# Kernel tuning notes

Measured on AMD Instinct MI355X. Metric: run time of the kernel, lower is better.

Reference implementation:

```python
import jax, jax.numpy as jnp
import numpy as np

EPS = 1e-6
D = 1152          # hidden_size
NH_HEADS = 16     # num_attention_heads
HD = D // NH_HEADS
INTER = 4304      # intermediate_size
H4 = 4 * D        # 4608
I4 = 4 * INTER    # 17216
B, H, W = 8, 64, 64
WH, WW = 2, 2


def setup_inputs() -> dict:
    key = jax.random.key(0)
    ks = jax.random.split(key, 12)
    s = 0.02
    inp = {
        "hidden_states": jax.random.normal(ks[0], (B, H * W, D), jnp.float32),
        "tgt_sizes": jnp.full((B, 2), 64, dtype=jnp.int32),
        "attention_mask": jnp.zeros((B, 1, 1, H * W), jnp.float32),
        "ln1_g": jnp.ones((D,), jnp.float32),
        "ln1_b": jnp.zeros((D,), jnp.float32),
        "qkv_w": jax.random.normal(ks[1], (D, 3 * D), jnp.float32) * s,
        "qkv_b": jnp.zeros((3 * D,), jnp.float32),
        "out_w": jax.random.normal(ks[2], (D, D), jnp.float32) * s,
        "out_b": jnp.zeros((D,), jnp.float32),
        "pre_g": jnp.ones((H4,), jnp.float32),
        "pre_b": jnp.zeros((H4,), jnp.float32),
        "w1": jax.random.normal(ks[3], (H4, I4), jnp.float32) * s,
        "b1": jnp.zeros((I4,), jnp.float32),
        "w2": jax.random.normal(ks[4], (I4, D), jnp.float32) * s,
        "b2": jnp.zeros((D,), jnp.float32),
    }
    return inp


def _layernorm(x, g, b):
    m = x.mean(-1, keepdims=True)
    v = ((x - m) ** 2).mean(-1, keepdims=True)
    return (x - m) * jax.lax.rsqrt(v + EPS) * g + b


def _partition(x):
    # x: [B, H*W, D] -> windows [B, nh*nw, wh*ww, D]
    nh, nw = H // WH, W // WW
    x = x.reshape(B, nh, WH, nw, WW, D)
    x = x.transpose(0, 1, 3, 2, 4, 5)  # [B, nh, nw, wh, ww, D]
    return x.reshape(B, nh * nw, WH * WW, D)


def _unpartition(x):
    # windows [B, nh*nw, wh*ww, D] -> [B, H*W, D]
    nh, nw = H // WH, W // WW
    x = x.reshape(B, nh, nw, WH, WW, D)
    x = x.transpose(0, 1, 3, 2, 4, 5)  # [B, nh, wh, nw, ww, D]
    return x.reshape(B, H * W, D)


def reference(hidden_states, tgt_sizes, attention_mask, ln1_g, ln1_b,
              qkv_w, qkv_b, out_w, out_b, pre_g, pre_b, w1, b1, w2, b2):
    nh, nw = H // WH, W // WW
    nwin = nh * nw
    residual = hidden_states
    hs = _layernorm(hidden_states, ln1_g, ln1_b)

    # window self-attention over 4-token windows
    xw = _partition(hs).reshape(B * nwin, WH * WW, D)
    qkv = xw @ qkv_w + qkv_b                               # [N, 4, 3D]
    q, k, v = jnp.split(qkv, 3, axis=-1)
    q = q.reshape(-1, WH * WW, NH_HEADS, HD)
    k = k.reshape(-1, WH * WW, NH_HEADS, HD)
    v = v.reshape(-1, WH * WW, NH_HEADS, HD)
    scale = HD ** -0.5
    scores = jnp.einsum('nqhd,nkhd->nhqk', q, k) * scale
    probs = jax.nn.softmax(scores, axis=-1)
    o = jnp.einsum('nhqk,nkhd->nqhd', probs, v).reshape(-1, WH * WW, D)
    o = o @ out_w + out_b
    attn_out = _unpartition(o.reshape(B, nwin, WH * WW, D))
    hs = residual + attn_out                               # [B, H*W, D]

    # MLP downsample over 2x2 windows
    xw = _partition(hs)                                    # [B, nwin, 4, D]
    res = xw.mean(axis=2)                                  # [B, nwin, D]
    xf = xw.reshape(B, nwin, WH * WW * D)                  # [B, nwin, 4D]
    xf = _layernorm(xf, pre_g, pre_b)
    xf = jax.nn.gelu(xf @ w1 + b1, approximate=True)
    xf = xf @ w2 + b2
    new_hidden = xf + res                                  # [B, nwin, D]

    new_tgt_sizes = tgt_sizes // 2
    # all samples fully valid -> mask of zeros (no -inf positions)
    min_val = jnp.finfo(new_hidden.dtype).min
    valid = jnp.arange(nwin)[None, :] < (new_tgt_sizes[:, 0] * new_tgt_sizes[:, 1])[:, None]
    new_attention_mask = ((~valid).astype(new_hidden.dtype) * min_val)[:, None, None, :]
    return new_hidden, new_tgt_sizes, new_attention_mask
```

## Files before the change

kernel.cpp:

```cpp
#include <hip/hip_runtime.h>
#include <cstdint>
#include <cstddef>

#define DEV __device__ __forceinline__
typedef unsigned short u16;
typedef unsigned int u32;
typedef short bf16x8 __attribute__((ext_vector_type(8)));
typedef float f32x4 __attribute__((ext_vector_type(4)));

typedef __attribute__((address_space(1))) u32 GU32;
typedef __attribute__((address_space(3))) u32 LU32;

DEV float bf2f(u16 v){ u32 x = ((u32)v)<<16; float f; __builtin_memcpy(&f,&x,4); return f; }
DEV u16 f2bf(float f){ u32 x; __builtin_memcpy(&x,&f,4); return (u16)((x + 0x7fffu + ((x>>16)&1u)) >> 16); }

DEV int map_row(int r){
  int b = r>>12, rr = r&4095;
  int win = rr>>2, t = rr&3;
  int wy = win>>5, wx = win&31;
  int y = (wy<<1) + (t>>1), x = (wx<<1) + (t&1);
  return (b<<12) + (y<<6) + x;
}

DEV void gl_lds16(const void* g, void* l){
  __builtin_amdgcn_global_load_lds((const GU32*)g, (LU32*)l, 16, 0, 0);
}

DEV void block_red2(float& s, float& ss, float* red){
  #pragma unroll
  for (int o=32;o;o>>=1){ s += __shfl_down(s,o); ss += __shfl_down(ss,o); }
  const int wv = threadIdx.x>>6;
  if ((threadIdx.x&63)==0){ red[wv*2]=s; red[wv*2+1]=ss; }
  __syncthreads();
  s  = red[0]+red[2]+red[4]+red[6];
  ss = red[1]+red[3]+red[5]+red[7];
}

__launch_bounds__(256)
__global__ void tconv_k(const float* __restrict__ W, u16* __restrict__ WT, int K, int N){
  __shared__ float tl[64][65];
  const int n0 = blockIdx.x << 6, k0 = blockIdx.y << 6;
  const int tx = threadIdx.x & 63, ty = threadIdx.x >> 6;
  #pragma unroll
  for (int rr = 0; rr < 64; rr += 4)
    tl[rr+ty][tx] = W[(size_t)(k0+rr+ty)*N + (n0+tx)];
  __syncthreads();
  #pragma unroll
  for (int rr = 0; rr < 64; rr += 4)
    WT[(size_t)(n0+rr+ty)*K + (k0+tx)] = f2bf(tl[tx][rr+ty]);
}

__launch_bounds__(256)
__global__ void ln1_k(const float* __restrict__ X, const float* __restrict__ g,
                      const float* __restrict__ b, u16* __restrict__ Y){
  __shared__ float red[8];
  const int r = blockIdx.x;
  const float* xr = X + (size_t)map_row(r)*1152;
  const int tid = threadIdx.x;
  const bool has2 = tid < 32;
  float4 v0 = ((const float4*)xr)[tid];
  float4 v1 = {0,0,0,0};
  float s  = v0.x+v0.y+v0.z+v0.w;
  float ss = v0.x*v0.x+v0.y*v0.y+v0.z*v0.z+v0.w*v0.w;
  if (has2){
    v1 = ((const float4*)xr)[tid+256];
    s  += v1.x+v1.y+v1.z+v1.w;
    ss += v1.x*v1.x+v1.y*v1.y+v1.z*v1.z+v1.w*v1.w;
  }
  block_red2(s, ss, red);
  const float mean = s*(1.0f/1152.0f);
  const float rstd = rsqrtf(ss*(1.0f/1152.0f) - mean*mean + 1e-6f);
  u16* yr = Y + (size_t)r*1152;
  {
    float4 gg = ((const float4*)g)[tid];
    float4 bb = ((const float4*)b)[tid];
    ushort4 o;
    o.x = f2bf((v0.x-mean)*rstd*gg.x + bb.x);
    o.y = f2bf((v0.y-mean)*rstd*gg.y + bb.y);
    o.z = f2bf((v0.z-mean)*rstd*gg.z + bb.z);
    o.w = f2bf((v0.w-mean)*rstd*gg.w + bb.w);
    *(ushort4*)(yr + tid*4) = o;
  }
  if (has2){
    float4 gg = ((const float4*)g)[tid+256];
    float4 bb = ((const float4*)b)[tid+256];
    ushort4 o;
    o.x = f2bf((v1.x-mean)*rstd*gg.x + bb.x);
    o.y = f2bf((v1.y-mean)*rstd*gg.y + bb.y);
    o.z = f2bf((v1.z-mean)*rstd*gg.z + bb.z);
    o.w = f2bf((v1.w-mean)*rstd*gg.w + bb.w);
    *(ushort4*)(yr + (tid+256)*4) = o;
  }
}

#define BAR()  asm volatile("s_barrier" ::: "memory")
#define VMW8() asm volatile("s_waitcnt vmcnt(8)" ::: "memory")
#define VMW4() asm volatile("s_waitcnt vmcnt(4)" ::: "memory")
#define VMW0() asm volatile("s_waitcnt vmcnt(0)" ::: "memory")
#define WNONE() do{}while(0)

template<int EPI>
__launch_bounds__(512, 1)
__global__ void gemm8p_k(const u16* __restrict__ A, const u16* __restrict__ BT,
                         int M, int N, int K, int lda, int ldb,
                         void* __restrict__ C, int ldc,
                         const float* __restrict__ bias,
                         const float* __restrict__ aux,
                         int nTM, int nTN)
{
  __shared__ __align__(16) u16 LS[2][2][2][8192];
  const int tid = threadIdx.x;
  const int lane = tid & 63;
  const int wave = tid >> 6;
  const int wr = wave >> 2, wc = wave & 3;

  const int bid  = blockIdx.x;
  const int band = 16 * nTN;
  const int bb   = bid / band, rr_ = bid % band;
  int mcnt = nTM - (bb<<4); if (mcnt > 16) mcnt = 16;
  const int mt = (bb<<4) + rr_ % mcnt;
  const int nt = rr_ / mcnt;
  const int m0 = mt << 8, n0 = nt << 8;

  const int lr1 = tid >> 3, sl = tid & 7;
  const int x_  = sl ^ (lr1 & 7);
  const int grow = ((x_ >> 2) << 7) + lr1;
  const int q_   = x_ & 3;
  const u16* aS = A  + (size_t)(m0 + grow)*lda + q_*8;
  const u16* bS = BT + (size_t)(n0 + grow)*ldb + q_*8;
  const size_t aR64 = (size_t)64*lda, bR64 = (size_t)64*ldb;

  const int l15 = lane & 15, l7 = lane & 7, qh = lane >> 4;
  const int aOff = l15*64 + ((((wr<<2)|qh) ^ l7) << 3);
  const int bOff = ((wc&1)<<12) + l15*64 + (((((wc>>1)<<2)|qh) ^ l7) << 3);

  f32x4 acc[8][4] = {};
  bf16x8 af[4], bv[4];
  const int NT = K >> 6;

#define ST(op_, db_, kh_, t_) do{ \
    const u16* src__ = (op_ ? bS : aS) + (size_t)(t_)*64 + (kh_)*32; \
    u16* dst__ = &LS[(db_)][(op_)][(kh_)][tid*8]; \
    gl_lds16(src__, dst__); \
    gl_lds16(src__ + (op_ ? bR64 : aR64), dst__ + 4096); \
  }while(0)

#define READA(db_, kh_, mh_) do{ \
    const u16* ap__ = &LS[(db_)][0][(kh_)][0] + aOff + ((mh_)?4096:0); \
    _Pragma("unroll") for (int i__=0;i__<4;i__++) af[i__] = *(const bf16x8*)(ap__ + i__*1024); \
  }while(0)

#define READB(db_, kh_) do{ \
    const u16* bp__ = &LS[(db_)][1][(kh_)][0] + bOff; \
    _Pragma("unroll") for (int i__=0;i__<4;i__++) bv[i__] = *(const bf16x8*)(bp__ + i__*1024); \
  }while(0)

#define MFMA16(B_) do{ \
    __builtin_amdgcn_s_setprio(1); \
    _Pragma("unroll") for (int i__=0;i__<4;i__++) \
      _Pragma("unroll") for (int n__=0;n__<4;n__++) \
        acc[(B_)+i__][n__] = __builtin_amdgcn_mfma_f32_16x16x32_bf16(af[i__], bv[n__], acc[(B_)+i__][n__], 0,0,0); \
    __builtin_amdgcn_s_setprio(0); \
  }while(0)

#define GROUP(t_, S01, S23, W1_, W3_) do{ \
    const int cb__ = (t_) & 1; \
    READA(cb__,0,0); READB(cb__,0); if (S01) ST(0, cb__^1, 1, (t_)+1); \
    MFMA16(0); \
    READA(cb__,0,1);                if (S01) ST(1, cb__^1, 1, (t_)+1); \
    MFMA16(4); \
    W1_(); BAR(); \
    READA(cb__,1,0); READB(cb__,1); if (S23) ST(0, cb__, 0, (t_)+2); \
    MFMA16(0); \
    READA(cb__,1,1);                if (S23) ST(1, cb__, 0, (t_)+2); \
    MFMA16(4); \
    W3_(); BAR(); \
  }while(0)

  ST(0,0,0,0); ST(1,0,0,0); ST(0,0,1,0); ST(1,0,1,0); ST(0,1,0,1); ST(1,1,0,1);
  VMW8(); BAR();

  int t = 0;
  for (; t < NT-2; ++t) GROUP(t, 1, 1, VMW8, VMW8);
  GROUP(t, 1, 0, VMW8, VMW4); ++t;
  GROUP(t, 0, 0, VMW0, WNONE);

#undef GROUP
#undef MFMA16
#undef READB
#undef READA
#undef ST

  #pragma unroll
  for (int mi=0;mi<8;mi++){
    const int row = m0 + (wr<<7) + (mi<<4) + ((lane>>4)<<2);
    #pragma unroll
    for (int ni=0;ni<4;ni++){
      const int col = n0 + (wc<<6) + (ni<<4) + (lane&15);
      if (col < N){
        const float bvv = bias[col];
        #pragma unroll
        for (int r2=0;r2<4;r2++){
          const int rw = row + r2;
          float v = acc[mi][ni][r2] + bvv;
          if (EPI==0){
            ((u16*)C)[(size_t)rw*ldc + col] = f2bf(v);
          } else if (EPI==1){
            v += aux[(size_t)map_row(rw)*ldc + col];
            ((u16*)C)[(size_t)rw*ldc + col] = f2bf(v);
          } else if (EPI==2){
            const float x = v;
            const float c = 0.7978845608028654f*(x + 0.044715f*x*x*x);
            v = 0.5f*x*(1.0f + tanhf(c));
            ((u16*)C)[(size_t)rw*ldc + col] = f2bf(v);
          } else {
            v += aux[(size_t)rw*ldc + col];
            ((float*)C)[(size_t)rw*ldc + col] = v;
          }
        }
      }
    }
  }
}

__launch_bounds__(256)
__global__ void attn_k(const u16* __restrict__ QKV, u16* __restrict__ O){
  const int wave = threadIdx.x >> 6, lane = threadIdx.x & 63;
  const int wg = blockIdx.x*4 + wave;
  const int t = lane >> 4, h = lane & 15;
  const u16* base = QKV + (size_t)wg*4*3456;

  float q[72];
  {
    const u16* qp = base + t*3456 + h*72;
    #pragma unroll
    for (int i=0;i<9;i++){
      bf16x8 v = *(const bf16x8*)(qp + i*8);
      #pragma unroll
      for (int j=0;j<8;j++) q[i*8+j] = bf2f((u16)v[j]);
    }
  }
  float sc[4];
  #pragma unroll
  for (int tp=0;tp<4;tp++){
    const u16* kp = base + tp*3456 + 1152 + h*72;
    float a = 0.f;
    #pragma unroll
    for (int i=0;i<9;i++){
      bf16x8 v = *(const bf16x8*)(kp + i*8);
      #pragma unroll
      for (int j=0;j<8;j++) a += q[i*8+j]*bf2f((u16)v[j]);
    }
    sc[tp] = a * 0.11785113019775793f;
  }
  const float mx = fmaxf(fmaxf(sc[0],sc[1]), fmaxf(sc[2],sc[3]));
  float p[4]; float sum = 0.f;
  #pragma unroll
  for (int tp=0;tp<4;tp++){ p[tp] = __expf(sc[tp]-mx); sum += p[tp]; }
  const float inv = 1.0f/sum;
  float o[72];
  #pragma unroll
  for (int i=0;i<72;i++) o[i] = 0.f;
  #pragma unroll
  for (int tp=0;tp<4;tp++){
    const float w = p[tp]*inv;
    const u16* vp = base + tp*3456 + 2304 + h*72;
    #pragma unroll
    for (int i=0;i<9;i++){
      bf16x8 v = *(const bf16x8*)(vp + i*8);
      #pragma unroll
      for (int j=0;j<8;j++) o[i*8+j] += w*bf2f((u16)v[j]);
    }
  }
  u16* op = O + (size_t)(wg*4+t)*1152 + h*72;
  #pragma unroll
  for (int i=0;i<9;i++){
    bf16x8 sv;
    #pragma unroll
    for (int j=0;j<8;j++) sv[j] = (short)f2bf(o[i*8+j]);
    *(bf16x8*)(op + i*8) = sv;
  }
}

__launch_bounds__(256)
__global__ void ln2res_k(const u16* __restrict__ hs2, const float* __restrict__ g,
                         const float* __restrict__ b, u16* __restrict__ Y,
                         float* __restrict__ res){
  __shared__ float buf[4608];
  __shared__ float red[8];
  const int w = blockIdx.x;
  const u16* xr = hs2 + (size_t)w*4608;
  float s = 0.f, ss = 0.f;
  for (int i = threadIdx.x*8; i < 4608; i += 2048){
    bf16x8 v = *(const bf16x8*)(xr + i);
    #pragma unroll
    for (int j=0;j<8;j++){
      float f = bf2f((u16)v[j]);
      buf[i+j] = f; s += f; ss += f*f;
    }
  }
  block_red2(s, ss, red);
  const float mean = s*(1.0f/4608.0f);
  const float rstd = rsqrtf(ss*(1.0f/4608.0f) - mean*mean + 1e-6f);
  u16* yr = Y + (size_t)w*4608;
  for (int i = threadIdx.x*8; i < 4608; i += 2048){
    bf16x8 sv;
    #pragma unroll
    for (int j=0;j<8;j++)
      sv[j] = (short)f2bf((buf[i+j]-mean)*rstd*g[i+j] + b[i+j]);
    *(bf16x8*)(yr + i) = sv;
  }
  for (int d = threadIdx.x; d < 1152; d += 256)
    res[(size_t)w*1152 + d] = 0.25f*(buf[d]+buf[d+1152]+buf[d+2304]+buf[d+3456]);
}

__global__ void tail_k(const int* __restrict__ tgt, float* __restrict__ out){
  const int tid = blockIdx.x*blockDim.x + threadIdx.x;
  float* t_out = out + 9437184;
  float* m_out = t_out + 16;
  if (tid < 16) t_out[tid] = (float)(tgt[tid] / 2);
  for (int i = tid; i < 8192; i += 256*32){
    const int b = i >> 10, w = i & 1023;
    const int lim = (tgt[b*2]/2) * (tgt[b*2+1]/2);
    m_out[i] = (w < lim) ? 0.0f : -3.40282346638528859812e+38f;
  }
}

extern "C" void kernel_launch(void* const* d_in, const int* in_sizes, int n_in,
                              void* d_out, int out_size, void* d_ws, size_t ws_size,
                              hipStream_t stream){
  const float* hidden = (const float*)d_in[0];
  const int*   tgt    = (const int*)  d_in[1];
  const float* ln1_g  = (const float*)d_in[3];
  const float* ln1_b  = (const float*)d_in[4];
  const float* qkv_w  = (const float*)d_in[5];
  const float* qkv_b  = (const float*)d_in[6];
  const float* out_w  = (const float*)d_in[7];
  const float* out_b  = (const float*)d_in[8];
  const float* pre_g  = (const float*)d_in[9];
  const float* pre_b  = (const float*)d_in[10];
  const float* w1     = (const float*)d_in[11];
  const float* b1     = (const float*)d_in[12];
  const float* w2     = (const float*)d_in[13];
  const float* b2     = (const float*)d_in[14];
  float* out = (float*)d_out;

  char* p = (char*)d_ws;
  auto alloc = [&](size_t bytes)->void*{ void* r = p; p += (bytes + 255) & ~(size_t)255; return r; };
  u16* w1T = (u16*)alloc(17216ull*4608*2);
  u16* w2T = (u16*)alloc(1152ull*17216*2);
  u16* wqT = (u16*)alloc(3456ull*1152*2);
  u16* woT = (u16*)alloc(1152ull*1152*2);
  u16* Xln = (u16*)alloc(32768ull*1152*2);
  char* qr = (char*)alloc(32768ull*3456*2);
  u16*   QKV  = (u16*)qr;
  u16*   hs2  = (u16*)qr;
  float* res  = (float*)(qr + 75497472);
  u16*   xfln = (u16*)(qr + 150994944);
  u16*   h1   = Xln;

  tconv_k<<<dim3(17216/64, 4608/64), 256, 0, stream>>>(w1, w1T, 4608, 17216);
  tconv_k<<<dim3(1152/64, 17216/64), 256, 0, stream>>>(w2, w2T, 17216, 1152);
  tconv_k<<<dim3(3456/64, 1152/64), 256, 0, stream>>>(qkv_w, wqT, 1152, 3456);
  tconv_k<<<dim3(1152/64, 1152/64), 256, 0, stream>>>(out_w, woT, 1152, 1152);
  ln1_k<<<32768, 256, 0, stream>>>(hidden, ln1_g, ln1_b, Xln);
  gemm8p_k<0><<<dim3(128*14), 512, 0, stream>>>(Xln, wqT, 32768, 3456, 1152, 1152, 1152,
                                                QKV, 3456, qkv_b, nullptr, 128, 14);
  attn_k<<<2048, 256, 0, stream>>>(QKV, Xln);
  gemm8p_k<1><<<dim3(128*5), 512, 0, stream>>>(Xln, woT, 32768, 1152, 1152, 1152, 1152,
                                               hs2, 1152, out_b, hidden, 128, 5);
  ln2res_k<<<8192, 256, 0, stream>>>(hs2, pre_g, pre_b, xfln, res);
  for (int r0 = 0; r0 < 8192; r0 += 4352){
    const int m = (8192 - r0 < 4352) ? (8192 - r0) : 4352;
    gemm8p_k<2><<<dim3((m>>8)*68), 512, 0, stream>>>(xfln + (size_t)r0*4608, w1T,
                                                     m, 17216, 4608, 4608, 4608,
                                                     h1, 17216, b1, nullptr, m>>8, 68);
    gemm8p_k<3><<<dim3((m>>8)*5), 512, 0, stream>>>(h1, w2T,
                                                    m, 1152, 17216, 17216, 17216,
                                                    out + (size_t)r0*1152, 1152, b2,
                                                    res + (size_t)r0*1152, m>>8, 5);
  }
  tail_k<<<32, 256, 0, stream>>>(tgt, out);
}
```

Baseline: 2.809 ms.

## Restructure GEMM main loop into four barrier-synchronized LDS-read/MFMA phases

Reorganizes each K-step of the bf16 MFMA GEMM into four phases, each issuing its LDS fragment reads, then a workgroup barrier, an explicit lgkmcnt(0) wait with a scheduling barrier, and an MFMA block. Global-to-LDS stores for the next tiles are redistributed across the phases, and vmcnt waits are retuned to match. The aim is to keep waves in lockstep so LDS reads and global loads interleave with MFMA work more predictably. The cost is twice as many barriers per iteration and forced full LDS waits, which could serialize work the compiler previously overlapped.

```diff
diff --git a/kernel.cpp b/kernel.cpp
--- a/kernel.cpp
+++ b/kernel.cpp
@@ -94,7 +94,10 @@
 }
 
 #define BAR()  asm volatile("s_barrier" ::: "memory")
+#define LGKM0() do{ asm volatile("s_waitcnt lgkmcnt(0)" ::: "memory"); \
+                    __builtin_amdgcn_sched_barrier(0); }while(0)
 #define VMW8() asm volatile("s_waitcnt vmcnt(8)" ::: "memory")
+#define VMW6() asm volatile("s_waitcnt vmcnt(6)" ::: "memory")
 #define VMW4() asm volatile("s_waitcnt vmcnt(4)" ::: "memory")
 #define VMW0() asm volatile("s_waitcnt vmcnt(0)" ::: "memory")
 #define WNONE() do{}while(0)
@@ -145,13 +148,13 @@
     gl_lds16(src__ + (op_ ? bR64 : aR64), dst__ + 4096); \
   }while(0)
 
-#define READA(db_, kh_, mh_) do{ \
-    const u16* ap__ = &LS[(db_)][0][(kh_)][0] + aOff + ((mh_)?4096:0); \
+#define READA(base_, mh_) do{ \
+    const u16* ap__ = (base_) + aOff + ((mh_)?4096:0); \
     _Pragma("unroll") for (int i__=0;i__<4;i__++) af[i__] = *(const bf16x8*)(ap__ + i__*1024); \
   }while(0)
 
-#define READB(db_, kh_) do{ \
-    const u16* bp__ = &LS[(db_)][1][(kh_)][0] + bOff; \
+#define READB(base_) do{ \
+    const u16* bp__ = (base_) + bOff; \
     _Pragma("unroll") for (int i__=0;i__<4;i__++) bv[i__] = *(const bf16x8*)(bp__ + i__*1024); \
   }while(0)
 
@@ -163,26 +166,32 @@
     __builtin_amdgcn_s_setprio(0); \
   }while(0)
 
-#define GROUP(t_, S01, S23, W1_, W3_) do{ \
+#define GROUP(t_, SE12, SE3, Wp1, Wp3) do{ \
     const int cb__ = (t_) & 1; \
-    READA(cb__,0,0); READB(cb__,0); if (S01) ST(0, cb__^1, 1, (t_)+1); \
-    MFMA16(0); \
-    READA(cb__,0,1);                if (S01) ST(1, cb__^1, 1, (t_)+1); \
-    MFMA16(4); \
-    W1_(); BAR(); \
-    READA(cb__,1,0); READB(cb__,1); if (S23) ST(0, cb__, 0, (t_)+2); \
-    MFMA16(0); \
-    READA(cb__,1,1);                if (S23) ST(1, cb__, 0, (t_)+2); \
-    MFMA16(4); \
-    W3_(); BAR(); \
+    const u16* rA0__ = &LS[cb__][0][0][0]; \
+    const u16* rB0__ = &LS[cb__][1][0][0]; \
+    const u16* rA1__ = &LS[cb__][0][1][0]; \
+    const u16* rB1__ = &LS[cb__][1][1][0]; \
+     \
+    READB(rB0__); READA(rA0__, 0); \
+    BAR(); LGKM0(); MFMA16(0); \
+     \
+    READA(rA0__, 1); if (SE12) ST(0, cb__^1, 1, (t_)+1); \
+    Wp1(); BAR(); LGKM0(); MFMA16(4); \
+     \
+    READB(rB1__); READA(rA1__, 0); if (SE12) ST(1, cb__^1, 1, (t_)+1); \
+    BAR(); LGKM0(); MFMA16(0); \
+     \
+    READA(rA1__, 1); if (SE3) { ST(0, cb__, 0, (t_)+2); ST(1, cb__, 0, (t_)+2); } \
+    Wp3(); BAR(); LGKM0(); MFMA16(4); \
   }while(0)
 
   ST(0,0,0,0); ST(1,0,0,0); ST(0,0,1,0); ST(1,0,1,0); ST(0,1,0,1); ST(1,1,0,1);
   VMW8(); BAR();
 
   int t = 0;
-  for (; t < NT-2; ++t) GROUP(t, 1, 1, VMW8, VMW8);
-  GROUP(t, 1, 0, VMW8, VMW4); ++t;
+  for (; t < NT-2; ++t) GROUP(t, 1, 1, VMW6, VMW8);
+  GROUP(t, 1, 0, VMW6, VMW4); ++t;
   GROUP(t, 0, 0, VMW0, WNONE);
 
 #undef GROUP
```

Result: no change. 2.824 ms (+0.5%).
